# Performance work log

Hardware: AMD Instinct MI355X
Metric: run time of the kernel (lower is better)

## Reference

```python
import jax, jax.numpy as jnp
import numpy as np

B, N, F_IN, F_HID, F_LAT = 32, 4096, 128, 64, 32


def setup_inputs() -> dict:
    key = jax.random.key(0)
    ks = jax.random.split(key, 7)
    x = jax.random.normal(ks[0], (B, N, F_IN), dtype=jnp.float32)
    q_ids = jax.random.randint(ks[1], (B,), 0, N)
    # dense (soft) adjacency, as stored on the module
    adj = jax.random.uniform(ks[2], (N, N), dtype=jnp.float32)
    W1 = jax.random.normal(ks[3], (F_IN, F_HID), dtype=jnp.float32) * 0.05
    b1 = jax.random.normal(ks[4], (F_HID,), dtype=jnp.float32) * 0.05
    W2 = jax.random.normal(ks[5], (F_HID, F_LAT), dtype=jnp.float32) * 0.05
    b2 = jax.random.normal(ks[6], (F_LAT,), dtype=jnp.float32) * 0.05
    return {"x": x, "q_ids": q_ids, "adj": adj, "W1": W1, "b1": b1, "W2": W2, "b2": b2}


def reference(x, q_ids, adj, W1, b1, W2, b2):
    # Layer 1 (batched, replaces the per-sample python loop):
    # gcn(x, adj) = adj @ (x @ W1) + b1, then relu
    support = jnp.einsum('bnf,fh->bnh', x, W1)          # (B, N, F_HID)
    h = jax.nn.relu(jnp.einsum('nm,bmh->bnh', adj, support) + b1)
    # Layer 2: each sample uses a single row adj[q_id] -> (1, N) aggregation
    rows = adj[q_ids]                                    # (B, N) gather
    agg = jnp.einsum('bn,bnh->bh', rows, h)              # (B, F_HID)
    out = agg @ W2 + b2                                  # (B, F_LAT), squeezed
    return out
```

## Files before the change

### kernel.cpp

```cpp
#include <hip/hip_runtime.h>
#include <hip/hip_bf16.h>
#include <stdint.h>

typedef __attribute__((ext_vector_type(4))) float f32x4;
typedef __attribute__((ext_vector_type(8))) short short8;

#define NN 4096
#define FIN 128
#define FHID 64
#define BATCH 32
#define NJ 2048

__device__ __forceinline__ unsigned short f2bf(float f) {
  unsigned u = __builtin_bit_cast(unsigned, f);
  u = (u + 0x7FFFu + ((u >> 16) & 1u)) >> 16;
  return (unsigned short)u;
}
__device__ __forceinline__ float bf2f(unsigned short h) {
  unsigned u = ((unsigned)h) << 16;
  return __builtin_bit_cast(float, u);
}
__device__ __forceinline__ void gload_lds16(const void* g, void* l) {
  __builtin_amdgcn_global_load_lds(
      (const __attribute__((address_space(1))) unsigned int*)g,
      (__attribute__((address_space(3))) unsigned int*)l, 16, 0, 0);
}

__global__ __launch_bounds__(256) void k_convert(const float* __restrict__ adj,
                                                 unsigned short* __restrict__ adjb) {
  long i = (long)blockIdx.x * 256 + threadIdx.x;
  const f32x4* in = (const f32x4*)adj;
  f32x4 v = in[i];
  ushort4 o;
  o.x = f2bf(v.x); o.y = f2bf(v.y); o.z = f2bf(v.z); o.w = f2bf(v.w);
  *(ushort4*)(adjb + i * 4) = o;
}

__global__ __launch_bounds__(256) void k_support(const float* __restrict__ x,
                                                 const float* __restrict__ W1,
                                                 unsigned short* __restrict__ St) {
  __shared__ unsigned short W1t[FHID * 136];
  __shared__ __align__(16) unsigned short T[FHID * 128];
  const int tid = threadIdx.x;
  for (int i = tid; i < FIN * FHID; i += 256) {
    int f = i >> 6, h = i & 63;
    W1t[h * 136 + f] = f2bf(W1[i]);
  }
  __syncthreads();

  const int bb = blockIdx.x >> 5;
  const int m0 = (blockIdx.x & 31) * 128;
  const int lane = tid & 63, wv = tid >> 6;
  const int fr = lane & 15, fq = lane >> 4;

  short8 bfr[4][4];
  #pragma unroll
  for (int ni = 0; ni < 4; ++ni)
    #pragma unroll
    for (int ks = 0; ks < 4; ++ks)
      bfr[ni][ks] = *(const short8*)&W1t[(ni * 16 + fr) * 136 + ks * 32 + fq * 8];

  const float* xr0 = x + ((size_t)bb * NN + m0 + wv * 32 + fr) * FIN;
  const float* xr1 = xr0 + (size_t)16 * FIN;

  f32x4 z = {0.f, 0.f, 0.f, 0.f};
  f32x4 acc[2][4];
  #pragma unroll
  for (int mf = 0; mf < 2; ++mf)
    #pragma unroll
    for (int ni = 0; ni < 4; ++ni) acc[mf][ni] = z;

  #pragma unroll
  for (int ks = 0; ks < 4; ++ks) {
    #pragma unroll
    for (int mf = 0; mf < 2; ++mf) {
      const float* src = (mf ? xr1 : xr0) + ks * 32 + fq * 8;
      f32x4 lo = *(const f32x4*)src;
      f32x4 hi = *(const f32x4*)(src + 4);
      short8 a;
      #pragma unroll
      for (int j = 0; j < 4; ++j) { a[j] = (short)f2bf(lo[j]); a[4 + j] = (short)f2bf(hi[j]); }
      #pragma unroll
      for (int ni = 0; ni < 4; ++ni)
        acc[mf][ni] = __builtin_amdgcn_mfma_f32_16x16x32_bf16(a, bfr[ni][ks], acc[mf][ni], 0, 0, 0);
    }
  }

  const int cr = (lane >> 4) * 4, cc = lane & 15;
  #pragma unroll
  for (int mf = 0; mf < 2; ++mf)
    #pragma unroll
    for (int ni = 0; ni < 4; ++ni) {
      ushort4 o;
      o.x = f2bf(acc[mf][ni][0]); o.y = f2bf(acc[mf][ni][1]);
      o.z = f2bf(acc[mf][ni][2]); o.w = f2bf(acc[mf][ni][3]);
      *(ushort4*)&T[(ni * 16 + cc) * 128 + wv * 32 + mf * 16 + cr] = o;
    }
  __syncthreads();
  for (int u = tid; u < FHID * 16; u += 256) {
    int row = u >> 4, ch = u & 15;
    *(short8*)(St + (size_t)(bb * FHID + row) * NN + m0 + ch * 8) =
        *(const short8*)&T[row * 128 + ch * 8];
  }
}

#define VMW(N)  asm volatile("s_waitcnt vmcnt(" #N ")" ::: "memory")
#define LGKM0   asm volatile("s_waitcnt lgkmcnt(0)" ::: "memory")
#define BAR     __builtin_amdgcn_s_barrier()

__global__ __launch_bounds__(256, 2) void k_gemm(const unsigned short* __restrict__ A,
                                                 const unsigned short* __restrict__ Bt,
                                                 const float* __restrict__ b1,
                                                 const float* __restrict__ adj,
                                                 const int* __restrict__ q_ids,
                                                 float* __restrict__ partial) {
  __shared__ __align__(16) unsigned short As[2 * 8192];
  __shared__ __align__(16) unsigned short Bs[2 * 8192];
  __shared__ float adjw[2][128];
  __shared__ float red[4][64];

  const int tid  = threadIdx.x;
  const int lane = tid & 63;
  const int wv   = tid >> 6;
  const int wm   = wv >> 1;
  const int wn   = wv & 1;
  const int bm   = blockIdx.x * 128;
  const int bn   = blockIdx.y * 128;
  const int fr   = lane & 15;
  const int fq   = lane >> 4;

  int offA[2][2][2], offB[4][2];
  #pragma unroll
  for (int h = 0; h < 2; ++h)
    #pragma unroll
    for (int m2 = 0; m2 < 2; ++m2) {
      int row = wm * 64 + h * 32 + m2 * 16 + fr;
      #pragma unroll
      for (int ks = 0; ks < 2; ++ks)
        offA[h][m2][ks] = row * 64 + ((((ks << 6) + (fq << 4)) ^ ((row & 7) << 4)) >> 1);
    }
  #pragma unroll
  for (int ni = 0; ni < 4; ++ni) {
    int row = wn * 64 + (ni >> 1) * 32 + (ni & 1) * 16 + fr;
    #pragma unroll
    for (int ks = 0; ks < 2; ++ks)
      offB[ni][ks] = row * 64 + ((((ks << 6) + (fq << 4)) ^ ((row & 7) << 4)) >> 1);
  }

  const int srow = tid >> 3;
  const int scol = ((((tid & 7) << 4) ^ ((srow & 7) << 4)) >> 1);
  const unsigned short* gA[4];
  const unsigned short* gB[4];
  #pragma unroll
  for (int c = 0; c < 4; ++c) {
    gA[c] = A  + (size_t)(bm + 32 * c + srow) * NN + scol;
    gB[c] = Bt + (size_t)(bn + 32 * c + srow) * NN + scol;
  }
  const int ld = tid * 8;

  f32x4 z = {0.f, 0.f, 0.f, 0.f};
  f32x4 acc[4][4];
  #pragma unroll
  for (int i = 0; i < 4; ++i)
    #pragma unroll
    for (int j = 0; j < 4; ++j) acc[i][j] = z;

  short8 av0[2][2], av1[2][2], bvB[2][2], bvA0[2][2], bvA1[2][2];

#define RD_AVA(Ac)                                                             \
    _Pragma("unroll") for (int m2 = 0; m2 < 2; ++m2)                           \
    _Pragma("unroll") for (int ks = 0; ks < 2; ++ks)                           \
      av0[m2][ks] = *(const short8*)((Ac) + offA[0][m2][ks]);
#define RD_AVB(Ac)                                                             \
    _Pragma("unroll") for (int m2 = 0; m2 < 2; ++m2)                           \
    _Pragma("unroll") for (int ks = 0; ks < 2; ++ks)                           \
      av1[m2][ks] = *(const short8*)((Ac) + offA[1][m2][ks]);
#define RD_BV(DST, Bb, P)                                                      \
    _Pragma("unroll") for (int n2 = 0; n2 < 2; ++n2)                           \
    _Pragma("unroll") for (int ks = 0; ks < 2; ++ks)                           \
      DST[n2][ks] = *(const short8*)((Bb) + offB[2 * (P) + n2][ks]);
#define MFMA8(MP, AV, BV, NP)                                                  \
    __builtin_amdgcn_s_setprio(1);                                             \
    _Pragma("unroll") for (int m2 = 0; m2 < 2; ++m2)                           \
    _Pragma("unroll") for (int n2 = 0; n2 < 2; ++n2)                           \
    _Pragma("unroll") for (int ks = 0; ks < 2; ++ks)                           \
      acc[2 * (MP) + m2][2 * (NP) + n2] = __builtin_amdgcn_mfma_f32_16x16x32_bf16( \
          AV[m2][ks], BV[n2][ks], acc[2 * (MP) + m2][2 * (NP) + n2], 0, 0, 0); \
    __builtin_amdgcn_s_setprio(0);
#define SG_A(C, KO, BUF) gload_lds16(gA[C] + (KO), As + (BUF) * 8192 + (C) * 2048 + ld);
#define SG_B(C, KO, BUF) gload_lds16(gB[C] + (KO), Bs + (BUF) * 8192 + (C) * 2048 + ld);

#define TILE(CUR, BVA_C, BVA_N, KQ, DOS, VMWOP) {                              \
    const unsigned short* Ac = As + (CUR) * 8192;                              \
    const unsigned short* Bc = Bs + (CUR) * 8192;                              \
    const unsigned short* Bn = Bs + (1 - (CUR)) * 8192;                        \
                                                               \
    RD_AVA(Ac)                                                                 \
    BAR; LGKM0;                                                                \
    MFMA8(0, av0, BVA_C, 0)                                                    \
                                       \
    RD_BV(bvB, Bc, 1)                                                          \
    if (DOS) { SG_A(0, KQ, CUR) SG_A(2, KQ, CUR)                               \
               SG_B(0, KQ, CUR) SG_B(2, KQ, CUR) }                             \
    BAR; LGKM0;                                                                \
    MFMA8(0, av0, bvB, 1)                                                      \
                                             \
    RD_AVB(Ac)                                                                 \
    if (DOS) { SG_B(1, KQ, CUR) SG_B(3, KQ, CUR) }                             \
    BAR; LGKM0;                                                                \
    MFMA8(1, av1, bvB, 1)                                                      \
          \
    VMWOP;                                                                     \
    if (DOS) { SG_A(1, KQ, CUR) SG_A(3, KQ, CUR) }                             \
    BAR;                                                                       \
    RD_BV(BVA_N, Bn, 0)                                                        \
    MFMA8(1, av1, BVA_C, 0)                                                    \
  }

  #pragma unroll
  for (int c = 0; c < 4; ++c) { SG_A(c, 0, 0) SG_B(c, 0, 0) }
  #pragma unroll
  for (int c = 0; c < 4; ++c) { SG_A(c, 64, 1) SG_B(c, 64, 1) }
  VMW(8);
  BAR;
  RD_BV(bvA0, Bs, 0)

  int kq = 128;
  #pragma unroll 1
  for (int g = 0; g < 31; ++g) {
    TILE(0, bvA0, bvA1, kq,      1, VMW(6))
    TILE(1, bvA1, bvA0, kq + 64, 1, VMW(6))
    kq += 128;
  }
  TILE(0, bvA0, bvA1, 0, 0, VMW(0))
  {
    const unsigned short* Ac = As + 8192;
    const unsigned short* Bc = Bs + 8192;
    RD_AVA(Ac)
    BAR; LGKM0;
    MFMA8(0, av0, bvA1, 0)
    RD_BV(bvB, Bc, 1)
    BAR; LGKM0;
    MFMA8(0, av0, bvB, 1)
    RD_AVB(Ac)
    BAR; LGKM0;
    MFMA8(1, av1, bvB, 1)
    MFMA8(1, av1, bvA1, 0)
  }
#undef RD_AVA
#undef RD_AVB
#undef RD_BV
#undef MFMA8
#undef SG_A
#undef SG_B
#undef TILE

  const int b0 = bn >> 6;
  {
    int bsel = tid >> 7;
    int rloc = tid & 127;
    adjw[bsel][rloc] = adj[(size_t)q_ids[b0 + bsel] * NN + bm + rloc];
  }
  __syncthreads();

  const int cr = (lane >> 4) * 4;
  const int cc = lane & 15;
  float ps[4];
  #pragma unroll
  for (int ni = 0; ni < 4; ++ni) {
    int colh = (ni >> 1) * 32 + (ni & 1) * 16 + cc;
    float bias = b1[colh];
    float s = 0.f;
    #pragma unroll
    for (int mi = 0; mi < 4; ++mi) {
      int rowl = wm * 64 + (mi >> 1) * 32 + (mi & 1) * 16 + cr;
      #pragma unroll
      for (int r = 0; r < 4; ++r) {
        float v = acc[mi][ni][r] + bias;
        v = v > 0.f ? v : 0.f;
        s += adjw[wn][rowl + r] * v;
      }
    }
    ps[ni] = s;
  }
  #pragma unroll
  for (int ni = 0; ni < 4; ++ni) {
    ps[ni] += __shfl_xor(ps[ni], 16, 64);
    ps[ni] += __shfl_xor(ps[ni], 32, 64);
  }
  if (lane < 16) {
    #pragma unroll
    for (int ni = 0; ni < 4; ++ni)
      red[wv][ni * 16 + cc] = ps[ni];
  }
  __syncthreads();
  if (tid < 128) {
    int wn2 = tid >> 6;
    int ni2 = (((tid >> 5) & 1) << 1) | ((tid >> 4) & 1);
    int sidx = ni2 * 16 + (tid & 15);
    float s = red[0 + wn2][sidx] + red[2 + wn2][sidx];
    partial[(size_t)blockIdx.x * NJ + bn + tid] = s;
  }
}

__global__ __launch_bounds__(1024) void k_out(const float* __restrict__ partial,
                                              const float* __restrict__ W2,
                                              const float* __restrict__ b2,
                                              float* __restrict__ out) {
  __shared__ float aggs[BATCH * FHID];
  int t = threadIdx.x;
  for (int idx = t; idx < BATCH * FHID; idx += 1024) {
    float s = 0.f;
    #pragma unroll
    for (int c = 0; c < 32; ++c) s += partial[c * NJ + idx];
    aggs[idx] = s;
  }
  __syncthreads();
  int b = t >> 5, l = t & 31;
  float o = b2[l];
  #pragma unroll
  for (int h = 0; h < FHID; ++h) o += aggs[b * FHID + h] * W2[h * 32 + l];
  out[b * 32 + l] = o;
}

extern "C" void kernel_launch(void* const* d_in, const int* in_sizes, int n_in,
                              void* d_out, int out_size, void* d_ws, size_t ws_size,
                              hipStream_t stream) {
  const float* x   = (const float*)d_in[0];
  const int*   q   = (const int*)d_in[1];
  const float* adj = (const float*)d_in[2];
  const float* W1  = (const float*)d_in[3];
  const float* b1  = (const float*)d_in[4];
  const float* W2  = (const float*)d_in[5];
  const float* b2  = (const float*)d_in[6];
  float* out = (float*)d_out;

  char* ws = (char*)d_ws;
  unsigned short* adjb   = (unsigned short*)ws;
  unsigned short* St     = (unsigned short*)(ws + (size_t)32 * 1024 * 1024);
  float*          partial= (float*)(ws + (size_t)48 * 1024 * 1024);

  k_convert<<<(NN * NN / 4) / 256, 256, 0, stream>>>(adj, adjb);
  k_support<<<1024, 256, 0, stream>>>(x, W1, St);
  dim3 g2(NN / 128, NJ / 128);
  k_gemm<<<g2, 256, 0, stream>>>(adjb, St, b1, adj, q, partial);
  k_out<<<1, 1024, 0, stream>>>(partial, W2, b2, out);
}
```

Measured before the change: 105.8 us.

## Fuse adj fp32-to-bf16 conversion into GEMM with 256x128 tiles and 512 threads

Drops the separate pass that converts the 64 MB fp32 adjacency to bf16. The GEMM now streams fp32 adj straight into LDS and packs it to bf16 at fragment-read time. The GEMM tile grows to 256x128 with 512 threads per block, and the grid becomes 256 blocks with a swizzled block mapping. This also halves the partial-sum rows that k_out has to reduce. In exchange, each k-step moves twice as many A bytes through global memory and LDS and adds VALU pack work inside the main loop, and fewer blocks run per CU.

New measurement: 130.9 us. 23.8% more time.

```diff
diff --git a/kernel.cpp b/kernel.cpp
--- a/kernel.cpp
+++ b/kernel.cpp
@@ -20,20 +20,19 @@
   unsigned u = ((unsigned)h) << 16;
   return __builtin_bit_cast(float, u);
 }
+__device__ __forceinline__ short8 pack8(f32x4 lo, f32x4 hi) {
+  short8 w;
+  #pragma unroll
+  for (int j = 0; j < 4; ++j) {
+    w[j]     = (short)f2bf(lo[j]);
+    w[4 + j] = (short)f2bf(hi[j]);
+  }
+  return w;
+}
 __device__ __forceinline__ void gload_lds16(const void* g, void* l) {
   __builtin_amdgcn_global_load_lds(
       (const __attribute__((address_space(1))) unsigned int*)g,
       (__attribute__((address_space(3))) unsigned int*)l, 16, 0, 0);
-}
-
-__global__ __launch_bounds__(256) void k_convert(const float* __restrict__ adj,
-                                                 unsigned short* __restrict__ adjb) {
-  long i = (long)blockIdx.x * 256 + threadIdx.x;
-  const f32x4* in = (const f32x4*)adj;
-  f32x4 v = in[i];
-  ushort4 o;
-  o.x = f2bf(v.x); o.y = f2bf(v.y); o.z = f2bf(v.z); o.w = f2bf(v.w);
-  *(ushort4*)(adjb + i * 4) = o;
 }
 
 __global__ __launch_bounds__(256) void k_support(const float* __restrict__ x,
@@ -77,9 +76,7 @@
       const float* src = (mf ? xr1 : xr0) + ks * 32 + fq * 8;
       f32x4 lo = *(const f32x4*)src;
       f32x4 hi = *(const f32x4*)(src + 4);
-      short8 a;
-      #pragma unroll
-      for (int j = 0; j < 4; ++j) { a[j] = (short)f2bf(lo[j]); a[4 + j] = (short)f2bf(hi[j]); }
+      short8 a = pack8(lo, hi);
       #pragma unroll
       for (int ni = 0; ni < 4; ++ni)
         acc[mf][ni] = __builtin_amdgcn_mfma_f32_16x16x32_bf16(a, bfr[ni][ks], acc[mf][ni], 0, 0, 0);
@@ -108,55 +105,64 @@
 #define LGKM0   asm volatile("s_waitcnt lgkmcnt(0)" ::: "memory")
 #define BAR     __builtin_amdgcn_s_barrier()
 
-__global__ __launch_bounds__(256, 2) void k_gemm(const unsigned short* __restrict__ A,
+__global__ __launch_bounds__(512, 1) void k_gemm(const float* __restrict__ Af,
                                                  const unsigned short* __restrict__ Bt,
                                                  const float* __restrict__ b1,
-                                                 const float* __restrict__ adj,
                                                  const int* __restrict__ q_ids,
                                                  float* __restrict__ partial) {
-  __shared__ __align__(16) unsigned short As[2 * 8192];
+  __shared__ __align__(16) float Asf[2 * 16384];
   __shared__ __align__(16) unsigned short Bs[2 * 8192];
-  __shared__ float adjw[2][128];
-  __shared__ float red[4][64];
 
   const int tid  = threadIdx.x;
   const int lane = tid & 63;
   const int wv   = tid >> 6;
   const int wm   = wv >> 1;
   const int wn   = wv & 1;
-  const int bm   = blockIdx.x * 128;
-  const int bn   = blockIdx.y * 128;
+  const int bid  = blockIdx.x;
+  const int xc   = bid & 7;
+  const int kk   = bid >> 3;
+  const int bx   = xc * 2 + (kk >> 4);
+  const int by   = kk & 15;
+  const int bm   = bx * 256;
+  const int bn   = by * 128;
   const int fr   = lane & 15;
   const int fq   = lane >> 4;
 
-  int offA[2][2][2], offB[4][2];
+  int offAF[2][2][2][2];
   #pragma unroll
   for (int h = 0; h < 2; ++h)
     #pragma unroll
     for (int m2 = 0; m2 < 2; ++m2) {
-      int row = wm * 64 + h * 32 + m2 * 16 + fr;
+      int row = wm * 32 + h * 128 + m2 * 16 + fr;
       #pragma unroll
       for (int ks = 0; ks < 2; ++ks)
-        offA[h][m2][ks] = row * 64 + ((((ks << 6) + (fq << 4)) ^ ((row & 7) << 4)) >> 1);
-    }
+        #pragma unroll
+        for (int hf = 0; hf < 2; ++hf) {
+          int byte = (ks * 128 + fq * 32 + hf * 16) ^ ((row & 15) << 4);
+          offAF[h][m2][ks][hf] = row * 64 + (byte >> 2);
+        }
+    }
+  int offB[4][2];
   #pragma unroll
   for (int ni = 0; ni < 4; ++ni) {
-    int row = wn * 64 + (ni >> 1) * 32 + (ni & 1) * 16 + fr;
+    int row = wn * 32 + (ni & 1) * 16 + (ni >> 1) * 64 + fr;
     #pragma unroll
     for (int ks = 0; ks < 2; ++ks)
       offB[ni][ks] = row * 64 + ((((ks << 6) + (fq << 4)) ^ ((row & 7) << 4)) >> 1);
   }
 
-  const int srow = tid >> 3;
-  const int scol = ((((tid & 7) << 4) ^ ((srow & 7) << 4)) >> 1);
-  const unsigned short* gA[4];
-  const unsigned short* gB[4];
-  #pragma unroll
-  for (int c = 0; c < 4; ++c) {
-    gA[c] = A  + (size_t)(bm + 32 * c + srow) * NN + scol;
-    gB[c] = Bt + (size_t)(bn + 32 * c + srow) * NN + scol;
-  }
-  const int ld = tid * 8;
+  const int srowA = tid >> 4;
+  const int scolA = ((((tid & 15) << 4) ^ ((srowA & 15) << 4)) >> 2);
+  const float* gAF[8];
+  #pragma unroll
+  for (int c = 0; c < 8; ++c)
+    gAF[c] = Af + (size_t)(bm + 32 * c + srowA) * NN + scolA;
+  const int ldA = tid * 4;
+  const int srowB = tid >> 3;
+  const int scolB = ((((tid & 7) << 4) ^ ((srowB & 7) << 4)) >> 1);
+  const unsigned short* gB0 = Bt + (size_t)(bn +  0 + srowB) * NN + scolB;
+  const unsigned short* gB1 = Bt + (size_t)(bn + 64 + srowB) * NN + scolB;
+  const int ldB = tid * 8;
 
   f32x4 z = {0.f, 0.f, 0.f, 0.f};
   f32x4 acc[4][4];
@@ -169,12 +175,18 @@
 
 #define RD_AVA(Ac)                                                             \
     _Pragma("unroll") for (int m2 = 0; m2 < 2; ++m2)                           \
-    _Pragma("unroll") for (int ks = 0; ks < 2; ++ks)                           \
-      av0[m2][ks] = *(const short8*)((Ac) + offA[0][m2][ks]);
+    _Pragma("unroll") for (int ks = 0; ks < 2; ++ks) {                         \
+      f32x4 lo = *(const f32x4*)((Ac) + offAF[0][m2][ks][0]);                  \
+      f32x4 hi = *(const f32x4*)((Ac) + offAF[0][m2][ks][1]);                  \
+      av0[m2][ks] = pack8(lo, hi);                                             \
+    }
 #define RD_AVB(Ac)                                                             \
     _Pragma("unroll") for (int m2 = 0; m2 < 2; ++m2)                           \
-    _Pragma("unroll") for (int ks = 0; ks < 2; ++ks)                           \
-      av1[m2][ks] = *(const short8*)((Ac) + offA[1][m2][ks]);
+    _Pragma("unroll") for (int ks = 0; ks < 2; ++ks) {                         \
+      f32x4 lo = *(const f32x4*)((Ac) + offAF[1][m2][ks][0]);                  \
+      f32x4 hi = *(const f32x4*)((Ac) + offAF[1][m2][ks][1]);                  \
+      av1[m2][ks] = pack8(lo, hi);                                             \
+    }
 #define RD_BV(DST, Bb, P)                                                      \
     _Pragma("unroll") for (int n2 = 0; n2 < 2; ++n2)                           \
     _Pragma("unroll") for (int ks = 0; ks < 2; ++ks)                           \
@@ -187,54 +199,59 @@
       acc[2 * (MP) + m2][2 * (NP) + n2] = __builtin_amdgcn_mfma_f32_16x16x32_bf16( \
           AV[m2][ks], BV[n2][ks], acc[2 * (MP) + m2][2 * (NP) + n2], 0, 0, 0); \
     __builtin_amdgcn_s_setprio(0);
-#define SG_A(C, KO, BUF) gload_lds16(gA[C] + (KO), As + (BUF) * 8192 + (C) * 2048 + ld);
-#define SG_B(C, KO, BUF) gload_lds16(gB[C] + (KO), Bs + (BUF) * 8192 + (C) * 2048 + ld);
+#define SG_AF(C, KO, BUF) gload_lds16(gAF[C] + (KO), Asf + (BUF) * 16384 + (C) * 2048 + ldA);
+#define SG_B0(KO, BUF)    gload_lds16(gB0 + (KO), Bs + (BUF) * 8192 + 0 * 4096 + ldB);
+#define SG_B1(KO, BUF)    gload_lds16(gB1 + (KO), Bs + (BUF) * 8192 + 1 * 4096 + ldB);
 
 #define TILE(CUR, BVA_C, BVA_N, KQ, DOS, VMWOP) {                              \
-    const unsigned short* Ac = As + (CUR) * 8192;                              \
+    const float* Ac = Asf + (CUR) * 16384;                                     \
     const unsigned short* Bc = Bs + (CUR) * 8192;                              \
     const unsigned short* Bn = Bs + (1 - (CUR)) * 8192;                        \
                                                                \
     RD_AVA(Ac)                                                                 \
     BAR; LGKM0;                                                                \
     MFMA8(0, av0, BVA_C, 0)                                                    \
-                                       \
+                                          \
     RD_BV(bvB, Bc, 1)                                                          \
-    if (DOS) { SG_A(0, KQ, CUR) SG_A(2, KQ, CUR)                               \
-               SG_B(0, KQ, CUR) SG_B(2, KQ, CUR) }                             \
+    if (DOS) { SG_AF(0, KQ, CUR) SG_AF(1, KQ, CUR)                             \
+               SG_AF(2, KQ, CUR) SG_AF(3, KQ, CUR) }                           \
     BAR; LGKM0;                                                                \
     MFMA8(0, av0, bvB, 1)                                                      \
-                                             \
+                                               \
     RD_AVB(Ac)                                                                 \
-    if (DOS) { SG_B(1, KQ, CUR) SG_B(3, KQ, CUR) }                             \
+    if (DOS) { SG_B1(KQ, CUR) }                                                \
     BAR; LGKM0;                                                                \
     MFMA8(1, av1, bvB, 1)                                                      \
-          \
+       \
     VMWOP;                                                                     \
-    if (DOS) { SG_A(1, KQ, CUR) SG_A(3, KQ, CUR) }                             \
+    if (DOS) { SG_AF(4, KQ, CUR) SG_AF(5, KQ, CUR)                             \
+               SG_AF(6, KQ, CUR) SG_AF(7, KQ, CUR)                             \
+               SG_B0(KQ, CUR) }                                                \
     BAR;                                                                       \
     RD_BV(BVA_N, Bn, 0)                                                        \
     MFMA8(1, av1, BVA_C, 0)                                                    \
   }
 
   #pragma unroll
-  for (int c = 0; c < 4; ++c) { SG_A(c, 0, 0) SG_B(c, 0, 0) }
-  #pragma unroll
-  for (int c = 0; c < 4; ++c) { SG_A(c, 64, 1) SG_B(c, 64, 1) }
-  VMW(8);
+  for (int c = 0; c < 8; ++c) { SG_AF(c, 0, 0) }
+  SG_B0(0, 0) SG_B1(0, 0)
+  #pragma unroll
+  for (int c = 0; c < 8; ++c) { SG_AF(c, 64, 1) }
+  SG_B0(64, 1) SG_B1(64, 1)
+  VMW(10);
   BAR;
   RD_BV(bvA0, Bs, 0)
 
   int kq = 128;
   #pragma unroll 1
   for (int g = 0; g < 31; ++g) {
-    TILE(0, bvA0, bvA1, kq,      1, VMW(6))
-    TILE(1, bvA1, bvA0, kq + 64, 1, VMW(6))
+    TILE(0, bvA0, bvA1, kq,      1, VMW(5))
+    TILE(1, bvA1, bvA0, kq + 64, 1, VMW(5))
     kq += 128;
   }
   TILE(0, bvA0, bvA1, 0, 0, VMW(0))
   {
-    const unsigned short* Ac = As + 8192;
+    const float* Ac = Asf + 16384;
     const unsigned short* Bc = Bs + 8192;
     RD_AVA(Ac)
     BAR; LGKM0;
@@ -251,15 +268,19 @@
 #undef RD_AVB
 #undef RD_BV
 #undef MFMA8
-#undef SG_A
-#undef SG_B
+#undef SG_AF
+#undef SG_B0
+#undef SG_B1
 #undef TILE
 
+  float* adjwF = (float*)Asf;
+  float* redF  = (float*)Asf + 512;
+  __syncthreads();
   const int b0 = bn >> 6;
   {
-    int bsel = tid >> 7;
-    int rloc = tid & 127;
-    adjw[bsel][rloc] = adj[(size_t)q_ids[b0 + bsel] * NN + bm + rloc];
+    int bsel = tid >> 8;
+    int rloc = tid & 255;
+    adjwF[bsel * 256 + rloc] = Af[(size_t)q_ids[b0 + bsel] * NN + bm + rloc];
   }
   __syncthreads();
 
@@ -268,17 +289,17 @@
   float ps[4];
   #pragma unroll
   for (int ni = 0; ni < 4; ++ni) {
-    int colh = (ni >> 1) * 32 + (ni & 1) * 16 + cc;
+    int colh = wn * 32 + (ni & 1) * 16 + cc;
     float bias = b1[colh];
     float s = 0.f;
     #pragma unroll
     for (int mi = 0; mi < 4; ++mi) {
-      int rowl = wm * 64 + (mi >> 1) * 32 + (mi & 1) * 16 + cr;
+      int rowl = wm * 32 + (mi & 1) * 16 + (mi >> 1) * 128 + cr;
       #pragma unroll
       for (int r = 0; r < 4; ++r) {
         float v = acc[mi][ni][r] + bias;
         v = v > 0.f ? v : 0.f;
-        s += adjw[wn][rowl + r] * v;
+        s += adjwF[(ni >> 1) * 256 + rowl + r] * v;
       }
     }
     ps[ni] = s;
@@ -291,15 +312,16 @@
   if (lane < 16) {
     #pragma unroll
     for (int ni = 0; ni < 4; ++ni)
-      red[wv][ni * 16 + cc] = ps[ni];
+      redF[(wm * 2 + wn) * 64 + ni * 16 + cc] = ps[ni];
   }
   __syncthreads();
   if (tid < 128) {
-    int wn2 = tid >> 6;
-    int ni2 = (((tid >> 5) & 1) << 1) | ((tid >> 4) & 1);
+    int wn2 = (tid >> 5) & 1;
+    int ni2 = ((tid >> 6) << 1) | ((tid >> 4) & 1);
     int sidx = ni2 * 16 + (tid & 15);
-    float s = red[0 + wn2][sidx] + red[2 + wn2][sidx];
-    partial[(size_t)blockIdx.x * NJ + bn + tid] = s;
+    float s = redF[(0 + wn2) * 64 + sidx] + redF[(2 + wn2) * 64 + sidx]
+            + redF[(4 + wn2) * 64 + sidx] + redF[(6 + wn2) * 64 + sidx];
+    partial[(size_t)bx * NJ + bn + tid] = s;
   }
 }
 
@@ -312,7 +334,7 @@
   for (int idx = t; idx < BATCH * FHID; idx += 1024) {
     float s = 0.f;
     #pragma unroll
-    for (int c = 0; c < 32; ++c) s += partial[c * NJ + idx];
+    for (int c = 0; c < 16; ++c) s += partial[c * NJ + idx];
     aggs[idx] = s;
   }
   __syncthreads();
@@ -336,13 +358,10 @@
   float* out = (float*)d_out;
 
   char* ws = (char*)d_ws;
-  unsigned short* adjb   = (unsigned short*)ws;
-  unsigned short* St     = (unsigned short*)(ws + (size_t)32 * 1024 * 1024);
-  float*          partial= (float*)(ws + (size_t)48 * 1024 * 1024);
-
-  k_convert<<<(NN * NN / 4) / 256, 256, 0, stream>>>(adj, adjb);
+  unsigned short* St     = (unsigned short*)ws;
+  float*          partial= (float*)(ws + (size_t)16 * 1024 * 1024);
+
   k_support<<<1024, 256, 0, stream>>>(x, W1, St);
-  dim3 g2(NN / 128, NJ / 128);
-  k_gemm<<<g2, 256, 0, stream>>>(adjb, St, b1, adj, q, partial);
+  k_gemm<<<256, 512, 0, stream>>>(adj, St, b1, q, partial);
   k_out<<<1, 1024, 0, stream>>>(partial, W2, b2, out);
 }
```
